# Kernel optimization log

Hardware: AMD Instinct MI355X
Metric: run time of the kernel (lower is better)

Reference implementation:

```python
import jax, jax.numpy as jnp
import numpy as np

D_MODEL = 512
NUM_HEADS = 8
D_K = D_MODEL // NUM_HEADS


def setup_inputs() -> dict:
    key = jax.random.key(0)
    ks = jax.random.split(key, 9)
    s = 1.0 / np.sqrt(D_MODEL)
    x = jax.random.normal(ks[0], (2, 4096, D_MODEL), dtype=jnp.float32)
    Wq = jax.random.uniform(ks[1], (D_MODEL, D_MODEL), jnp.float32, -s, s)
    bq = jax.random.uniform(ks[2], (D_MODEL,), jnp.float32, -s, s)
    Wk = jax.random.uniform(ks[3], (D_MODEL, D_MODEL), jnp.float32, -s, s)
    bk = jax.random.uniform(ks[4], (D_MODEL,), jnp.float32, -s, s)
    Wv = jax.random.uniform(ks[5], (D_MODEL, D_MODEL), jnp.float32, -s, s)
    bv = jax.random.uniform(ks[6], (D_MODEL,), jnp.float32, -s, s)
    Wo = jax.random.uniform(ks[7], (D_MODEL, D_MODEL), jnp.float32, -s, s)
    bo = jax.random.uniform(ks[8], (D_MODEL,), jnp.float32, -s, s)
    return {"x": x, "Wq": Wq, "bq": bq, "Wk": Wk, "bk": bk,
            "Wv": Wv, "bv": bv, "Wo": Wo, "bo": bo}


def reference(x, Wq, bq, Wk, bk, Wv, bv, Wo, bo):
    B, S, _ = x.shape
    # projections; split heads -> [B, H, S, d_k]
    def heads(t):
        return t.reshape(B, S, NUM_HEADS, D_K).transpose(0, 2, 1, 3)
    Q = heads(x @ Wq + bq)
    K = heads(x @ Wk + bk)
    V = heads(x @ Wv + bv)
    scores = jnp.einsum('bhqd,bhkd->bhqk', Q, K) / jnp.sqrt(jnp.float32(D_K))
    attn = jax.nn.softmax(scores, axis=-1)
    out = jnp.einsum('bhqk,bhkd->bhqd', attn, V)
    out = out.transpose(0, 2, 1, 3).reshape(B, S, D_MODEL)
    return out @ Wo + bo
```

## Files before the change

kernel.cpp:

```cpp
#include <hip/hip_runtime.h>
#include <hip/hip_bf16.h>

#define S_LEN 4096
#define DMODEL 512
#define NHEADS 8
#define DK 64
#define BATCH 2
#define MROWS (BATCH * S_LEN)

typedef __attribute__((ext_vector_type(8))) short bf16x8;
typedef __attribute__((ext_vector_type(4))) float f32x4;
typedef unsigned short ushort_t;

__device__ __forceinline__ unsigned packbf(float a, float b) {
  union { __hip_bfloat16 h; unsigned short s; } ua, ub;
  ua.h = __float2bfloat16(a);
  ub.h = __float2bfloat16(b);
  return (unsigned)ua.s | ((unsigned)ub.s << 16);
}

__device__ __forceinline__ unsigned short bf1(float a) {
  union { __hip_bfloat16 h; unsigned short s; } u;
  u.h = __float2bfloat16(a);
  return u.s;
}

__device__ __forceinline__ void gll16(const void* g, void* l) {
  __builtin_amdgcn_global_load_lds(
      (const __attribute__((address_space(1))) unsigned*)g,
      (__attribute__((address_space(3))) unsigned*)l, 16, 0, 0);
}

__global__ __launch_bounds__(256) void cvt_bf16(const float* __restrict__ in,
                                                ushort_t* __restrict__ out) {
  size_t i = ((size_t)blockIdx.x * 256 + threadIdx.x) * 8;
  float4 a = *reinterpret_cast<const float4*>(in + i);
  float4 b = *reinterpret_cast<const float4*>(in + i + 4);
  uint4 o;
  o.x = packbf(a.x, a.y);
  o.y = packbf(a.z, a.w);
  o.z = packbf(b.x, b.y);
  o.w = packbf(b.z, b.w);
  *reinterpret_cast<uint4*>(out + i) = o;
}

__global__ __launch_bounds__(256) void transp_w(const float* __restrict__ W,
                                                ushort_t* __restrict__ Wt) {
  __shared__ float T[32][33];
  const int tid = threadIdx.x;
  const int k0 = blockIdx.x * 32, n0 = blockIdx.y * 32;
  const int r = tid >> 3, c4 = (tid & 7) * 4;
  float4 v = *reinterpret_cast<const float4*>(W + (size_t)(k0 + r) * 512 + n0 + c4);
  T[r][c4 + 0] = v.x; T[r][c4 + 1] = v.y; T[r][c4 + 2] = v.z; T[r][c4 + 3] = v.w;
  __syncthreads();
  uint2 o;
  o.x = packbf(T[c4 + 0][r], T[c4 + 1][r]);
  o.y = packbf(T[c4 + 2][r], T[c4 + 3][r]);
  *reinterpret_cast<uint2*>(Wt + (size_t)(n0 + r) * 512 + k0 + c4) = o;
}

__global__ __launch_bounds__(256) void gemm_qkv(
    const ushort_t* __restrict__ A, const ushort_t* __restrict__ Wcat,
    const float* __restrict__ bq, const float* __restrict__ bk,
    const float* __restrict__ bv, ushort_t* __restrict__ Qo,
    ushort_t* __restrict__ Ko, ushort_t* __restrict__ Vo, float CQ) {
  __shared__ ushort_t AL[2][128 * 32];
  __shared__ ushort_t BL[2][128 * 32];
  const int tid = threadIdx.x;
  const int wid = tid >> 6;
  const int lane = tid & 63;
  const int ql = lane & 15;
  const int g = lane >> 4;
  const int wr = wid >> 1, wc = wid & 1;
  const int m0 = blockIdx.x * 128, n0 = blockIdx.y * 128;
  const int region = n0 >> 9;

  f32x4 acc[4][4];
#pragma unroll
  for (int i = 0; i < 4; ++i)
#pragma unroll
    for (int j = 0; j < 4; ++j) acc[i][j] = (f32x4){0.f, 0.f, 0.f, 0.f};

  auto stage = [&](int k0, int buf) {
#pragma unroll
    for (int i = 0; i < 2; ++i) {
      int idx = i * 256 + tid;
      int r = idx >> 2;
      int c = (idx & 3) * 8;
      gll16(A + (size_t)(m0 + r) * 512 + k0 + c, &AL[buf][idx * 8]);
      gll16(Wcat + (size_t)(n0 + r) * 512 + k0 + c, &BL[buf][idx * 8]);
    }
  };

  stage(0, 0);
  __syncthreads();
  int buf = 0;

  for (int t = 0; t < 16; ++t) {
    if (t < 15) stage((t + 1) * 32, buf ^ 1);
    const ushort_t* ALb = &AL[buf][0];
    const ushort_t* BLb = &BL[buf][0];
    bf16x8 af[4], bfr[4];
#pragma unroll
    for (int mi = 0; mi < 4; ++mi)
      af[mi] = *reinterpret_cast<const bf16x8*>(ALb + (wr * 64 + mi * 16 + ql) * 32 + g * 8);
#pragma unroll
    for (int ni = 0; ni < 4; ++ni)
      bfr[ni] = *reinterpret_cast<const bf16x8*>(BLb + (wc * 64 + ni * 16 + ql) * 32 + g * 8);
#pragma unroll
    for (int mi = 0; mi < 4; ++mi)
#pragma unroll
      for (int ni = 0; ni < 4; ++ni)
        acc[mi][ni] = __builtin_amdgcn_mfma_f32_16x16x32_bf16(af[mi], bfr[ni], acc[mi][ni], 0, 0, 0);
    __syncthreads();
    buf ^= 1;
  }

  const float* bias = region == 0 ? bq : (region == 1 ? bk : bv);
  const float scale = region == 0 ? CQ : 1.0f;
  const int nl0 = n0 - (region << 9);
  ushort_t* outT = region == 0 ? Qo : Ko;

  float bvv[4];
#pragma unroll
  for (int ni = 0; ni < 4; ++ni) bvv[ni] = bias[nl0 + wc * 64 + ni * 16 + ql];

#pragma unroll
  for (int mi = 0; mi < 4; ++mi) {
#pragma unroll
    for (int ni = 0; ni < 4; ++ni) {
      int nl = nl0 + wc * 64 + ni * 16 + ql;
      int h = nl >> 6, d = nl & 63;
#pragma unroll
      for (int reg = 0; reg < 4; ++reg) {
        float val = (acc[mi][ni][reg] + bvv[ni]) * scale;
        int m = m0 + wr * 64 + mi * 16 + 4 * g + reg;
        int b = m >> 12, s = m & 4095;
        if (region <= 1) {
          outT[(((size_t)(b * NHEADS + h) * S_LEN + s) * DK) + d] = bf1(val);
        } else {
          Vo[(((size_t)(b * NHEADS + h) * DK + d) * S_LEN) + s] = bf1(val);
        }
      }
    }
  }
}

__global__ __launch_bounds__(256) void gemm_wo(
    const ushort_t* __restrict__ A, const ushort_t* __restrict__ Wt,
    const float* __restrict__ bias, float* __restrict__ out) {
  __shared__ ushort_t AL[2][128 * 32];
  __shared__ ushort_t BL[2][128 * 32];
  const int tid = threadIdx.x;
  const int wid = tid >> 6;
  const int lane = tid & 63;
  const int ql = lane & 15;
  const int g = lane >> 4;
  const int wr = wid >> 1, wc = wid & 1;
  const int m0 = blockIdx.x * 128, n0 = blockIdx.y * 128;

  f32x4 acc[4][4];
#pragma unroll
  for (int i = 0; i < 4; ++i)
#pragma unroll
    for (int j = 0; j < 4; ++j) acc[i][j] = (f32x4){0.f, 0.f, 0.f, 0.f};

  auto stage = [&](int k0, int buf) {
#pragma unroll
    for (int i = 0; i < 2; ++i) {
      int idx = i * 256 + tid;
      int r = idx >> 2;
      int c = (idx & 3) * 8;
      gll16(A + (size_t)(m0 + r) * 512 + k0 + c, &AL[buf][idx * 8]);
      gll16(Wt + (size_t)(n0 + r) * 512 + k0 + c, &BL[buf][idx * 8]);
    }
  };

  stage(0, 0);
  __syncthreads();
  int buf = 0;

  for (int t = 0; t < 16; ++t) {
    if (t < 15) stage((t + 1) * 32, buf ^ 1);
    const ushort_t* ALb = &AL[buf][0];
    const ushort_t* BLb = &BL[buf][0];
    bf16x8 af[4], bfr[4];
#pragma unroll
    for (int mi = 0; mi < 4; ++mi)
      af[mi] = *reinterpret_cast<const bf16x8*>(ALb + (wr * 64 + mi * 16 + ql) * 32 + g * 8);
#pragma unroll
    for (int ni = 0; ni < 4; ++ni)
      bfr[ni] = *reinterpret_cast<const bf16x8*>(BLb + (wc * 64 + ni * 16 + ql) * 32 + g * 8);
#pragma unroll
    for (int mi = 0; mi < 4; ++mi)
#pragma unroll
      for (int ni = 0; ni < 4; ++ni)
        acc[mi][ni] = __builtin_amdgcn_mfma_f32_16x16x32_bf16(af[mi], bfr[ni], acc[mi][ni], 0, 0, 0);
    __syncthreads();
    buf ^= 1;
  }

  float bv[4];
#pragma unroll
  for (int ni = 0; ni < 4; ++ni) bv[ni] = bias[n0 + wc * 64 + ni * 16 + ql];

#pragma unroll
  for (int mi = 0; mi < 4; ++mi) {
#pragma unroll
    for (int ni = 0; ni < 4; ++ni) {
      int n = n0 + wc * 64 + ni * 16 + ql;
#pragma unroll
      for (int reg = 0; reg < 4; ++reg) {
        int m = m0 + wr * 64 + mi * 16 + 4 * g + reg;
        out[(size_t)m * 512 + n] = acc[mi][ni][reg] + bv[ni];
      }
    }
  }
}

template <bool SPLIT2>
__global__ __launch_bounds__(256, 4) void attn_mfma(
    const ushort_t* __restrict__ Q, const ushort_t* __restrict__ K,
    const ushort_t* __restrict__ Vt, ushort_t* __restrict__ AO,
    float* __restrict__ Opart, float* __restrict__ Lpart) {
  __shared__ ushort_t KL[2][64 * 64];
  __shared__ ushort_t VL[2][64 * 64];

  const int tid = threadIdx.x;
  const int wid = tid >> 6;
  const int lane = tid & 63;
  const int g = lane >> 4;
  const int ql = lane & 15;

  int L;
  if (SPLIT2) {
    int orig = blockIdx.x;
    L = (orig & 7) * 128 + (orig >> 3);
  } else {
    L = blockIdx.x;
  }
  const int qt = L & 31;
  const int bhsp = L >> 5;
  const int sp = SPLIT2 ? (bhsp & 1) : 0;
  const int bh = SPLIT2 ? (bhsp >> 1) : bhsp;
  const int NT = SPLIT2 ? 32 : 64;
  const int t0 = sp * NT;

  const ushort_t* Qb = Q + (size_t)bh * S_LEN * DK;
  const ushort_t* Kb = K + (size_t)bh * S_LEN * DK;
  const ushort_t* Vb = Vt + (size_t)bh * DK * S_LEN;

  const int qbase = qt * 128 + wid * 32;

  bf16x8 qf[2][2];
#pragma unroll
  for (int c = 0; c < 2; ++c) {
    int q = qbase + c * 16 + ql;
#pragma unroll
    for (int t = 0; t < 2; ++t)
      qf[c][t] = *reinterpret_cast<const bf16x8*>(Qb + (size_t)q * DK + t * 32 + g * 8);
  }

  bf16x8 ones;
#pragma unroll
  for (int j = 0; j < 8; ++j) ones[j] = (short)0x3F80;

  f32x4 ot[4][2];
#pragma unroll
  for (int db = 0; db < 4; ++db)
#pragma unroll
    for (int c = 0; c < 2; ++c) ot[db][c] = (f32x4){0.f, 0.f, 0.f, 0.f};
  f32x4 lacc[2];
  lacc[0] = (f32x4){0.f, 0.f, 0.f, 0.f};
  lacc[1] = (f32x4){0.f, 0.f, 0.f, 0.f};

  const int srow = lane >> 3;
  const int schk = lane & 7;
  const int r0 = wid * 16 + srow;
  const int r1 = r0 + 8;
  const int ssc = (schk ^ srow) << 4;

  const char* gk0 = (const char*)Kb + ((size_t)(t0 * 64 + r0)) * 128 + ssc;
  const char* gk1 = (const char*)Kb + ((size_t)(t0 * 64 + r1)) * 128 + ssc;
  const char* gv0 = (const char*)Vb + (size_t)r0 * (S_LEN * 2) + (size_t)t0 * 128 + ssc;
  const char* gv1 = (const char*)Vb + (size_t)r1 * (S_LEN * 2) + (size_t)t0 * 128 + ssc;

  char* lkA0 = (char*)&KL[0][0] + r0 * 128 + (schk << 4) - (srow << 4) + (lane & 7) * 16;
  lkA0 = (char*)&KL[0][0] + (wid * 16) * 128 + lane * 16;
  char* lkB0 = lkA0 + 8 * 128;
  char* lkA1 = lkA0 + 8192;
  char* lkB1 = lkB0 + 8192;
  char* lvA0 = (char*)&VL[0][0] + (wid * 16) * 128 + lane * 16;
  char* lvB0 = lvA0 + 8 * 128;
  char* lvA1 = lvA0 + 8192;
  char* lvB1 = lvB0 + 8192;

  int koA[4], koB[4];
#pragma unroll
  for (int kb = 0; kb < 4; ++kb) {
    int r = kb * 16 + ql;
    koA[kb] = r * 128 + (((g) ^ (r & 7)) << 4);
    koB[kb] = r * 128 + (((g + 4) ^ (r & 7)) << 4);
  }
  const int intra = (g & 1) << 3;
  int voL[2][4], voH[2][4];
#pragma unroll
  for (int t = 0; t < 2; ++t)
#pragma unroll
    for (int db = 0; db < 4; ++db) {
      int rd = db * 16 + ql;
      int c1 = t * 4 + (g >> 1);
      voL[t][db] = rd * 128 + ((c1 ^ (rd & 7)) << 4) + intra;
      voH[t][db] = rd * 128 + (((c1 + 2) ^ (rd & 7)) << 4) + intra;
    }

  gll16(gk0, lkA0); gll16(gk1, lkB0);
  gll16(gv0, lvA0); gll16(gv1, lvB0);
  gk0 += 8192; gk1 += 8192; gv0 += 128; gv1 += 128;
  __syncthreads();

  auto body = [&](const char* KB, const char* VB, char* dkA, char* dkB,
                  char* dvA, char* dvB, bool pref) {
    if (pref) {
      gll16(gk0, dkA); gll16(gk1, dkB);
      gll16(gv0, dvA); gll16(gv1, dvB);
      gk0 += 8192; gk1 += 8192; gv0 += 128; gv1 += 128;
    }

    f32x4 st[4][2];
    __builtin_amdgcn_s_setprio(1);
#pragma unroll
    for (int kb = 0; kb < 4; ++kb) {
      bf16x8 k0 = *reinterpret_cast<const bf16x8*>(KB + koA[kb]);
      bf16x8 k1 = *reinterpret_cast<const bf16x8*>(KB + koB[kb]);
#pragma unroll
      for (int c = 0; c < 2; ++c) {
        f32x4 z = (f32x4){0.f, 0.f, 0.f, 0.f};
        z = __builtin_amdgcn_mfma_f32_16x16x32_bf16(k0, qf[c][0], z, 0, 0, 0);
        z = __builtin_amdgcn_mfma_f32_16x16x32_bf16(k1, qf[c][1], z, 0, 0, 0);
        st[kb][c] = z;
      }
    }
    __builtin_amdgcn_s_setprio(0);

    unsigned pk[2][4][2];
#pragma unroll
    for (int c = 0; c < 2; ++c)
#pragma unroll
      for (int kb = 0; kb < 4; ++kb)
#pragma unroll
        for (int r2 = 0; r2 < 2; ++r2) {
          float pa = __builtin_amdgcn_exp2f(st[kb][c][2 * r2]);
          float pb_ = __builtin_amdgcn_exp2f(st[kb][c][2 * r2 + 1]);
          pk[c][kb][r2] = packbf(pa, pb_);
        }

    __builtin_amdgcn_s_setprio(1);
#pragma unroll
    for (int t = 0; t < 2; ++t) {
      union { unsigned u[4]; bf16x8 v; } pb0, pb1;
      pb0.u[0] = pk[0][2 * t][0];     pb0.u[1] = pk[0][2 * t][1];
      pb0.u[2] = pk[0][2 * t + 1][0]; pb0.u[3] = pk[0][2 * t + 1][1];
      pb1.u[0] = pk[1][2 * t][0];     pb1.u[1] = pk[1][2 * t][1];
      pb1.u[2] = pk[1][2 * t + 1][0]; pb1.u[3] = pk[1][2 * t + 1][1];
#pragma unroll
      for (int db = 0; db < 4; ++db) {
        uint2 lo = *reinterpret_cast<const uint2*>(VB + voL[t][db]);
        uint2 hi = *reinterpret_cast<const uint2*>(VB + voH[t][db]);
        union { unsigned u[4]; bf16x8 v; } af;
        af.u[0] = lo.x; af.u[1] = lo.y; af.u[2] = hi.x; af.u[3] = hi.y;
        ot[db][0] = __builtin_amdgcn_mfma_f32_16x16x32_bf16(af.v, pb0.v, ot[db][0], 0, 0, 0);
        ot[db][1] = __builtin_amdgcn_mfma_f32_16x16x32_bf16(af.v, pb1.v, ot[db][1], 0, 0, 0);
      }
      lacc[0] = __builtin_amdgcn_mfma_f32_16x16x32_bf16(ones, pb0.v, lacc[0], 0, 0, 0);
      lacc[1] = __builtin_amdgcn_mfma_f32_16x16x32_bf16(ones, pb1.v, lacc[1], 0, 0, 0);
    }
    __builtin_amdgcn_s_setprio(0);

    __syncthreads();
  };

  const char* KB0 = (const char*)&KL[0][0];
  const char* VB0 = (const char*)&VL[0][0];
  const char* KB1 = (const char*)&KL[1][0];
  const char* VB1 = (const char*)&VL[1][0];

  for (int it = 0; it < NT; it += 2) {
    body(KB0, VB0, lkA1, lkB1, lvA1, lvB1, true);
    body(KB1, VB1, lkA0, lkB0, lvA0, lvB0, it + 2 < NT);
  }

  if (SPLIT2) {
    float* Ob = Opart + (((size_t)sp * 16 + bh) * S_LEN) * 64;
#pragma unroll
    for (int c = 0; c < 2; ++c) {
      const int q = qbase + c * 16 + ql;
#pragma unroll
      for (int db = 0; db < 4; ++db) {
        float4 o = make_float4(ot[db][c][0], ot[db][c][1], ot[db][c][2], ot[db][c][3]);
        *reinterpret_cast<float4*>(Ob + (size_t)q * 64 + db * 16 + 4 * g) = o;
      }
      if (g == 0) Lpart[((size_t)sp * 16 + bh) * S_LEN + q] = lacc[c][0];
    }
  } else {
    const int b = bh >> 3, h = bh & 7;
#pragma unroll
    for (int c = 0; c < 2; ++c) {
      const int q = qbase + c * 16 + ql;
      float inv = 1.f / lacc[c][0];
#pragma unroll
      for (int db = 0; db < 4; ++db) {
        uint2 o;
        o.x = packbf(ot[db][c][0] * inv, ot[db][c][1] * inv);
        o.y = packbf(ot[db][c][2] * inv, ot[db][c][3] * inv);
        *reinterpret_cast<uint2*>(AO + ((size_t)b * S_LEN + q) * DMODEL + h * DK + db * 16 + g * 4) = o;
      }
    }
  }
}

__global__ __launch_bounds__(256) void combine_o(
    const float* __restrict__ Opart, const float* __restrict__ Lpart,
    ushort_t* __restrict__ AO) {
  int idx = blockIdx.x * 256 + threadIdx.x;
  int dblk = idx & 7;
  int q = (idx >> 3) & 4095;
  int bh = idx >> 15;
  size_t o0 = ((size_t)bh * S_LEN + q) * 64 + dblk * 8;
  size_t o1 = o0 + (size_t)16 * S_LEN * 64;
  float4 a0 = *reinterpret_cast<const float4*>(Opart + o0);
  float4 b0 = *reinterpret_cast<const float4*>(Opart + o0 + 4);
  float4 a1 = *reinterpret_cast<const float4*>(Opart + o1);
  float4 b1 = *reinterpret_cast<const float4*>(Opart + o1 + 4);
  float l = Lpart[(size_t)bh * S_LEN + q] + Lpart[(size_t)(16 + bh) * S_LEN + q];
  float inv = 1.0f / l;
  int b = bh >> 3, h = bh & 7;
  uint4 o;
  o.x = packbf((a0.x + a1.x) * inv, (a0.y + a1.y) * inv);
  o.y = packbf((a0.z + a1.z) * inv, (a0.w + a1.w) * inv);
  o.z = packbf((b0.x + b1.x) * inv, (b0.y + b1.y) * inv);
  o.w = packbf((b0.z + b1.z) * inv, (b0.w + b1.w) * inv);
  *reinterpret_cast<uint4*>(AO + ((size_t)b * S_LEN + q) * DMODEL + h * 64 + dblk * 8) = o;
}

extern "C" void kernel_launch(void* const* d_in, const int* in_sizes, int n_in,
                              void* d_out, int out_size, void* d_ws, size_t ws_size,
                              hipStream_t stream) {
  const float* x  = (const float*)d_in[0];
  const float* Wq = (const float*)d_in[1];
  const float* bq = (const float*)d_in[2];
  const float* Wk = (const float*)d_in[3];
  const float* bk = (const float*)d_in[4];
  const float* Wv = (const float*)d_in[5];
  const float* bv = (const float*)d_in[6];
  const float* Wo = (const float*)d_in[7];
  const float* bo = (const float*)d_in[8];
  float* out = (float*)d_out;

  const float CQ = 0.18033688f;

  char* ws = (char*)d_ws;
  const size_t NBF = (size_t)MROWS * DMODEL;
  ushort_t* xbf = (ushort_t*)ws;
  ushort_t* Qbf = (ushort_t*)(ws + NBF * 2);
  ushort_t* Kbf = (ushort_t*)(ws + NBF * 4);
  ushort_t* Vtb = (ushort_t*)(ws + NBF * 6);

  const size_t OFF_WT    = NBF * 8;
  const size_t OFF_LPART = OFF_WT + 4 * 512 * 512 * 2;
  const size_t OFF_OPART = OFF_LPART + 512 * 1024;
  const size_t NEED_SPLIT = OFF_OPART + (size_t)2 * 16 * S_LEN * 64 * 4;
  const bool use_split = ws_size >= NEED_SPLIT;

  ushort_t* Wcat;
  ushort_t* AOb;
  if (use_split) {
    Wcat = (ushort_t*)(ws + OFF_WT);
    AOb = xbf;
  } else {
    AOb = (ushort_t*)(ws + NBF * 8);
    Wcat = (ushort_t*)(ws + NBF * 10);
  }
  ushort_t* Wot = Wcat + 3 * 512 * 512;
  float* Lpart = (float*)(ws + OFF_LPART);
  float* Opart = (float*)(ws + OFF_OPART);

  cvt_bf16<<<MROWS * DMODEL / 2048, 256, 0, stream>>>(x, xbf);
  dim3 gt(16, 16);
  transp_w<<<gt, 256, 0, stream>>>(Wq, Wcat);
  transp_w<<<gt, 256, 0, stream>>>(Wk, Wcat + 512 * 512);
  transp_w<<<gt, 256, 0, stream>>>(Wv, Wcat + 2 * 512 * 512);
  transp_w<<<gt, 256, 0, stream>>>(Wo, Wot);

  dim3 gq(MROWS / 128, 1536 / 128);
  gemm_qkv<<<gq, 256, 0, stream>>>(xbf, Wcat, bq, bk, bv, Qbf, Kbf, Vtb, CQ);

  if (use_split) {
    attn_mfma<true><<<1024, 256, 0, stream>>>(Qbf, Kbf, Vtb, AOb, Opart, Lpart);
    combine_o<<<2048, 256, 0, stream>>>(Opart, Lpart, AOb);
  } else {
    attn_mfma<false><<<512, 256, 0, stream>>>(Qbf, Kbf, Vtb, AOb, Opart, Lpart);
  }

  dim3 gg(MROWS / 128, DMODEL / 128);
  gemm_wo<<<gg, 256, 0, stream>>>(AOb, Wot, bo, out);
}
```

Before: 139.9 us.

## Permute V token order at projection so PV loads become single 16-byte LDS reads

The QKV projection epilogue now writes V^T with the token index permuted inside each 64-token block. The attention kernel can then fetch each MFMA A-operand with one 128-bit LDS read instead of two 64-bit reads plus repacking. It also swaps the software bf16 pair conversion for the hardware v_cvt_pk_bf16_f32 instruction. The permutation has to match the MFMA k-lane mapping exactly, or the PV product will be wrong.

```diff
diff --git a/kernel.cpp b/kernel.cpp
--- a/kernel.cpp
+++ b/kernel.cpp
@@ -13,10 +13,9 @@
 typedef unsigned short ushort_t;
 
 __device__ __forceinline__ unsigned packbf(float a, float b) {
-  union { __hip_bfloat16 h; unsigned short s; } ua, ub;
-  ua.h = __float2bfloat16(a);
-  ub.h = __float2bfloat16(b);
-  return (unsigned)ua.s | ((unsigned)ub.s << 16);
+  unsigned r;
+  asm("v_cvt_pk_bf16_f32 %0, %1, %2" : "=v"(r) : "v"(a), "v"(b));
+  return r;
 }
 
 __device__ __forceinline__ unsigned short bf1(float a) {
@@ -139,7 +138,10 @@
         if (region <= 1) {
           outT[(((size_t)(b * NHEADS + h) * S_LEN + s) * DK) + d] = bf1(val);
         } else {
-          Vo[(((size_t)(b * NHEADS + h) * DK + d) * S_LEN) + s] = bf1(val);
+          int k6 = s & 63;
+          int pos = (k6 & 32) | (((k6 >> 2) & 3) << 3) | (((k6 >> 4) & 1) << 2) | (k6 & 3);
+          int sperm = (s & ~63) | pos;
+          Vo[(((size_t)(b * NHEADS + h) * DK + d) * S_LEN) + sperm] = bf1(val);
         }
       }
     }
@@ -285,8 +287,7 @@
   const char* gv0 = (const char*)Vb + (size_t)r0 * (S_LEN * 2) + (size_t)t0 * 128 + ssc;
   const char* gv1 = (const char*)Vb + (size_t)r1 * (S_LEN * 2) + (size_t)t0 * 128 + ssc;
 
-  char* lkA0 = (char*)&KL[0][0] + r0 * 128 + (schk << 4) - (srow << 4) + (lane & 7) * 16;
-  lkA0 = (char*)&KL[0][0] + (wid * 16) * 128 + lane * 16;
+  char* lkA0 = (char*)&KL[0][0] + (wid * 16) * 128 + lane * 16;
   char* lkB0 = lkA0 + 8 * 128;
   char* lkA1 = lkA0 + 8192;
   char* lkB1 = lkB0 + 8192;
@@ -302,16 +303,13 @@
     koA[kb] = r * 128 + (((g) ^ (r & 7)) << 4);
     koB[kb] = r * 128 + (((g + 4) ^ (r & 7)) << 4);
   }
-  const int intra = (g & 1) << 3;
-  int voL[2][4], voH[2][4];
+  int voP[2][4];
 #pragma unroll
   for (int t = 0; t < 2; ++t)
 #pragma unroll
     for (int db = 0; db < 4; ++db) {
       int rd = db * 16 + ql;
-      int c1 = t * 4 + (g >> 1);
-      voL[t][db] = rd * 128 + ((c1 ^ (rd & 7)) << 4) + intra;
-      voH[t][db] = rd * 128 + (((c1 + 2) ^ (rd & 7)) << 4) + intra;
+      voP[t][db] = rd * 128 + (((t * 4 + g) ^ (rd & 7)) << 4);
     }
 
   gll16(gk0, lkA0); gll16(gk1, lkB0);
@@ -365,12 +363,9 @@
       pb1.u[2] = pk[1][2 * t + 1][0]; pb1.u[3] = pk[1][2 * t + 1][1];
 #pragma unroll
       for (int db = 0; db < 4; ++db) {
-        uint2 lo = *reinterpret_cast<const uint2*>(VB + voL[t][db]);
-        uint2 hi = *reinterpret_cast<const uint2*>(VB + voH[t][db]);
-        union { unsigned u[4]; bf16x8 v; } af;
-        af.u[0] = lo.x; af.u[1] = lo.y; af.u[2] = hi.x; af.u[3] = hi.y;
-        ot[db][0] = __builtin_amdgcn_mfma_f32_16x16x32_bf16(af.v, pb0.v, ot[db][0], 0, 0, 0);
-        ot[db][1] = __builtin_amdgcn_mfma_f32_16x16x32_bf16(af.v, pb1.v, ot[db][1], 0, 0, 0);
+        bf16x8 af = *reinterpret_cast<const bf16x8*>(VB + voP[t][db]);
+        ot[db][0] = __builtin_amdgcn_mfma_f32_16x16x32_bf16(af, pb0.v, ot[db][0], 0, 0, 0);
+        ot[db][1] = __builtin_amdgcn_mfma_f32_16x16x32_bf16(af, pb1.v, ot[db][1], 0, 0, 0);
       }
       lacc[0] = __builtin_amdgcn_mfma_f32_16x16x32_bf16(ones, pb0.v, lacc[0], 0, 0, 0);
       lacc[1] = __builtin_amdgcn_mfma_f32_16x16x32_bf16(ones, pb1.v, lacc[1], 0, 0, 0);
```

After: 127.9 us. 8.6% less time.
